# Optimization experiments

Measured on AMD Instinct MI355X. Metric: run time of the kernel, lower is better.

Reference implementation:

```python
import jax, jax.numpy as jnp
import numpy as np

B, N, DIM, H, DH, MLP, DEPTH = 32, 256, 384, 6, 64, 1536, 12
INNER = H * DH
LN_EPS = 1e-5
LS_INIT = 0.1  # LayerScale init_eps for depth <= 18


def setup_inputs() -> dict:
    key = jax.random.key(0)
    ks = jax.random.split(key, 10)
    f = lambda k, shape, s=0.02: jax.random.normal(k, shape, jnp.float32) * s
    return {
        "x": jax.random.normal(ks[0], (B, N, DIM), jnp.float32),
        "ln1_g": jnp.ones((DEPTH, DIM), jnp.float32),
        "ln1_b": jnp.zeros((DEPTH, DIM), jnp.float32),
        "wq": f(ks[1], (DEPTH, DIM, INNER)),
        "wkv": f(ks[2], (DEPTH, DIM, 2 * INNER)),
        "scale": jnp.full((DEPTH, H), DH ** -0.5, jnp.float32),  # learned per-head scale
        "mix_pre": f(ks[3], (DEPTH, H, H), 1.0),   # torch.randn init
        "mix_post": f(ks[4], (DEPTH, H, H), 1.0),
        "wo": f(ks[5], (DEPTH, INNER, DIM)),
        "bo": jnp.zeros((DEPTH, DIM), jnp.float32),
        "ls1": jnp.full((DEPTH, DIM), LS_INIT, jnp.float32),
        "ln2_g": jnp.ones((DEPTH, DIM), jnp.float32),
        "ln2_b": jnp.zeros((DEPTH, DIM), jnp.float32),
        "w1": f(ks[6], (DEPTH, DIM, MLP)),
        "b1": jnp.zeros((DEPTH, MLP), jnp.float32),
        "w2": f(ks[7], (DEPTH, MLP, DIM)),
        "b2": jnp.zeros((DEPTH, DIM), jnp.float32),
        "ls2": jnp.full((DEPTH, DIM), LS_INIT, jnp.float32),
    }


def _layernorm(x, g, b):
    mu = jnp.mean(x, axis=-1, keepdims=True)
    var = jnp.mean(jnp.square(x - mu), axis=-1, keepdims=True)
    return (x - mu) * jax.lax.rsqrt(var + LN_EPS) * g + b


def reference(x, ln1_g, ln1_b, wq, wkv, scale, mix_pre, mix_post, wo, bo, ls1,
              ln2_g, ln2_b, w1, b1, w2, b2, ls2):
    diag = jnp.eye(N, dtype=bool)  # self-attention diagonal mask

    def block(x, p):
        (g1, bb1, wq_, wkv_, sc, mp, mq, wo_, bo_, l1,
         g2, bb2, w1_, b1_, w2_, b2_, l2) = p
        # --- talking-heads attention (PreNorm + LayerScale + residual) ---
        y = _layernorm(x, g1, bb1)
        q = (y @ wq_).reshape(B, N, H, DH).transpose(0, 2, 1, 3)       # b h n d
        kv = y @ wkv_
        k, v = jnp.split(kv, 2, axis=-1)
        k = k.reshape(B, N, H, DH).transpose(0, 2, 1, 3)
        v = v.reshape(B, N, H, DH).transpose(0, 2, 1, 3)
        dots = jnp.einsum('bhid,bhjd->bhij', q, k) * sc[None, :, None, None]
        dots = jnp.einsum('bhij,hg->bgij', dots, mp)                   # pre-softmax head mix
        dots = jnp.where(diag, -jnp.inf, dots)                         # mask self positions
        attn = jax.nn.softmax(dots, axis=-1)
        attn = jnp.einsum('bhij,hg->bgij', attn, mq)                   # post-softmax head mix
        o = jnp.einsum('bhij,bhjd->bhid', attn, v)
        o = o.transpose(0, 2, 1, 3).reshape(B, N, INNER) @ wo_ + bo_
        x = o * l1 + x
        # --- FFN (PreNorm + LayerScale + residual) ---
        y2 = _layernorm(x, g2, bb2)
        h = jax.nn.gelu(y2 @ w1_ + b1_, approximate=False)
        x = (h @ w2_ + b2_) * l2 + x
        return x, None

    params = (ln1_g, ln1_b, wq, wkv, scale, mix_pre, mix_post, wo, bo, ls1,
              ln2_g, ln2_b, w1, b1, w2, b2, ls2)
    x, _ = jax.lax.scan(block, x, params)
    return x
```

## Files before the change

kernel.cpp:

```cpp
#include <hip/hip_runtime.h>
#include <hip/hip_bf16.h>
#include <math.h>

#define B_ 32
#define N_ 256
#define DIM_ 384
#define H_ 6
#define DH_ 64
#define INNER_ 384
#define MLP_ 1536
#define DEPTH_ 12
#define T_ (B_ * N_)

typedef __bf16 bf16x8 __attribute__((ext_vector_type(8)));
typedef __bf16 bf16x4 __attribute__((ext_vector_type(4)));
typedef float f32x4 __attribute__((ext_vector_type(4)));

#define WQKV_OFF 0
#define WO_OFF   (1152 * 384)
#define W1_OFF   (WO_OFF + 384 * 384)
#define W2_OFF   (W1_OFF + 1536 * 384)
#define WBUF_ELEMS (W2_OFF + 384 * 1536)

__global__ __launch_bounds__(256) void convert_w(
    const float* __restrict__ wq, const float* __restrict__ wkv,
    const float* __restrict__ wo, const float* __restrict__ w1,
    const float* __restrict__ w2, __bf16* __restrict__ wbuf)
{
    __shared__ float til[64][65];
    int t = blockIdx.x;
    int lane = threadIdx.x & 63, seg = threadIdx.x >> 6;
    const float* src; __bf16* dst;
    int Ns, sc, dK, dR, k0;
    if (t < 108) {
        int nt = t / 6, kt = t % 6;
        int n0 = nt * 64; k0 = kt * 64;
        dst = wbuf + WQKV_OFF; dK = 384; dR = n0;
        if (n0 < 384) { src = wq;  Ns = 384; sc = n0; }
        else          { src = wkv; Ns = 768; sc = n0 - 384; }
    } else if (t < 144) {
        int u = t - 108; int nt = u / 6, kt = u % 6;
        src = wo; Ns = 384; sc = nt * 64;
        dst = wbuf + WO_OFF; dK = 384; dR = nt * 64; k0 = kt * 64;
    } else if (t < 288) {
        int u = t - 144; int nt = u / 6, kt = u % 6;
        src = w1; Ns = 1536; sc = nt * 64;
        dst = wbuf + W1_OFF; dK = 384; dR = nt * 64; k0 = kt * 64;
    } else {
        int u = t - 288; int nt = u / 24, kt = u % 24;
        src = w2; Ns = 384; sc = nt * 64;
        dst = wbuf + W2_OFF; dK = 1536; dR = nt * 64; k0 = kt * 64;
    }
    #pragma unroll
    for (int r = 0; r < 16; ++r) {
        int i = seg * 16 + r;
        til[i][lane] = src[(size_t)(k0 + i) * Ns + sc + lane];
    }
    __syncthreads();
    #pragma unroll
    for (int r = 0; r < 16; ++r) {
        int i = seg * 16 + r;
        dst[(size_t)(dR + i) * dK + k0 + lane] = (__bf16)til[lane][i];
    }
}

__global__ __launch_bounds__(64) void ln1w(
    const float* __restrict__ x, const float* __restrict__ g,
    const float* __restrict__ b, __bf16* __restrict__ y)
{
    size_t row = blockIdx.x;
    int lane = threadIdx.x;
    const float* xr = x + row * DIM_;
    float v[6];
    #pragma unroll
    for (int s = 0; s < 6; ++s) v[s] = xr[lane + 64 * s];
    float sum = 0.f;
    #pragma unroll
    for (int s = 0; s < 6; ++s) sum += v[s];
    #pragma unroll
    for (int o = 32; o > 0; o >>= 1) sum += __shfl_xor(sum, o);
    float mu = sum * (1.0f / DIM_);
    float var = 0.f;
    #pragma unroll
    for (int s = 0; s < 6; ++s) { float d = v[s] - mu; var += d * d; }
    #pragma unroll
    for (int o = 32; o > 0; o >>= 1) var += __shfl_xor(var, o);
    float rs = rsqrtf(var * (1.0f / DIM_) + 1e-5f);
    __bf16* yr = y + row * DIM_;
    #pragma unroll
    for (int s = 0; s < 6; ++s) {
        int e = lane + 64 * s;
        yr[e] = (__bf16)((v[s] - mu) * rs * g[e] + b[e]);
    }
}

#define LDK 40

template<int MODE, int K>
__global__ __launch_bounds__(256) void gemm128(
    const __bf16* __restrict__ A, const __bf16* __restrict__ Bt,
    const float* __restrict__ bias, const float* __restrict__ ls,
    float* __restrict__ xf, __bf16* __restrict__ out,
    __bf16* __restrict__ oq, __bf16* __restrict__ ok, __bf16* __restrict__ ov,
    int Nn)
{
    __shared__ __bf16 sA[2][128 * LDK];
    __shared__ __bf16 sB[2][128 * LDK];
    int id = blockIdx.x;
    int g = id & 7, j = id >> 3;
    int bm = (g + ((j & 7) << 3)) << 7;
    int bn = (j >> 3) << 7;
    int tid = threadIdx.x;
    int lane = tid & 63, wid = tid >> 6;
    int wm = (wid & 1) * 64, wn = (wid >> 1) * 64;
    int fm = lane & 15, fq = lane >> 4;

    f32x4 acc[4][4] = {};

    int sr = tid >> 1, sh = (tid & 1) << 4;
    const __bf16* aSrc = A + (size_t)(bm + sr) * K + sh;
    const __bf16* bSrc = Bt + (size_t)(bn + sr) * K + sh;
    int soff = sr * LDK + sh;

    constexpr int nIter = K >> 5;

    {
        bf16x8 a0 = *(const bf16x8*)(aSrc);
        bf16x8 a1 = *(const bf16x8*)(aSrc + 8);
        bf16x8 b0 = *(const bf16x8*)(bSrc);
        bf16x8 b1 = *(const bf16x8*)(bSrc + 8);
        *(bf16x8*)&sA[0][soff]     = a0;
        *(bf16x8*)&sA[0][soff + 8] = a1;
        *(bf16x8*)&sB[0][soff]     = b0;
        *(bf16x8*)&sB[0][soff + 8] = b1;
    }
    bf16x8 pa0 = *(const bf16x8*)(aSrc + 32);
    bf16x8 pa1 = *(const bf16x8*)(aSrc + 40);
    bf16x8 pb0 = *(const bf16x8*)(bSrc + 32);
    bf16x8 pb1 = *(const bf16x8*)(bSrc + 40);
    __syncthreads();

    #pragma unroll
    for (int i = 0; i < nIter; ++i) {
        int cur = i & 1, nxt = cur ^ 1;
        bf16x8 af[4], bf[4];
        #pragma unroll
        for (int ii = 0; ii < 4; ++ii)
            af[ii] = *(const bf16x8*)&sA[cur][(wm + ii * 16 + fm) * LDK + fq * 8];
        #pragma unroll
        for (int jj = 0; jj < 4; ++jj)
            bf[jj] = *(const bf16x8*)&sB[cur][(wn + jj * 16 + fm) * LDK + fq * 8];
        if (i + 1 < nIter) {
            *(bf16x8*)&sA[nxt][soff]     = pa0;
            *(bf16x8*)&sA[nxt][soff + 8] = pa1;
            *(bf16x8*)&sB[nxt][soff]     = pb0;
            *(bf16x8*)&sB[nxt][soff + 8] = pb1;
        }
        if (i + 2 < nIter) {
            int ko = (i + 2) << 5;
            pa0 = *(const bf16x8*)(aSrc + ko);
            pa1 = *(const bf16x8*)(aSrc + ko + 8);
            pb0 = *(const bf16x8*)(bSrc + ko);
            pb1 = *(const bf16x8*)(bSrc + ko + 8);
        }
        #pragma unroll
        for (int ii = 0; ii < 4; ++ii)
            #pragma unroll
            for (int jj = 0; jj < 4; ++jj)
                acc[ii][jj] = __builtin_amdgcn_mfma_f32_16x16x32_bf16(af[ii], bf[jj], acc[ii][jj], 0, 0, 0);
        if (i + 1 < nIter) __syncthreads();
    }

    #pragma unroll
    for (int jj = 0; jj < 4; ++jj) {
        int col = bn + wn + jj * 16 + fm;
        float bv = (MODE != 0) ? bias[col] : 0.0f;
        float lv = (MODE == 2) ? ls[col] : 0.0f;
        #pragma unroll
        for (int i = 0; i < 4; ++i) {
            #pragma unroll
            for (int r = 0; r < 4; ++r) {
                int row = bm + wm + i * 16 + fq * 4 + r;
                float v = acc[i][jj][r];
                if (MODE == 0) {
                    if (col < 384)      oq[(size_t)row * 384 + col] = (__bf16)v;
                    else if (col < 768) ok[(size_t)row * 384 + col - 384] = (__bf16)v;
                    else {
                        int bb = row >> 8, tj = row & 255;
                        ov[((size_t)bb * 384 + (col - 768)) * 256 + tj] = (__bf16)v;
                    }
                } else if (MODE == 1) {
                    v += bv;
                    v = 0.5f * v * (1.0f + erff(v * 0.70710678118f));
                    out[(size_t)row * Nn + col] = (__bf16)v;
                } else {
                    size_t idx = (size_t)row * Nn + col;
                    xf[idx] = (v + bv) * lv + xf[idx];
                }
            }
        }
    }
}

#define PAD_S 264

__global__ __launch_bounds__(384) void attn_mfma(
    const __bf16* __restrict__ q, const __bf16* __restrict__ kb,
    const __bf16* __restrict__ vT, const float* __restrict__ scale,
    const float* __restrict__ mp, const float* __restrict__ mq,
    __bf16* __restrict__ o)
{
    __shared__ __bf16 sbuf[96][PAD_S];
    __shared__ float smp[36], smq[36];

    int id = blockIdx.x;
    int b = (id & 7) + ((id >> 3) & 3) * 8;
    int i0 = (id >> 5) * 16;
    int tid = threadIdx.x;
    int lane = tid & 63, wid = tid >> 6;
    int fm = lane & 15, fq = lane >> 4;

    if (tid < 36) {
        smp[tid] = mp[tid] * scale[tid / 6];
        smq[tid] = mq[tid];
    }

    int h = wid;
    bf16x8 qf[2];
    #pragma unroll
    for (int ks = 0; ks < 2; ++ks)
        qf[ks] = *(const bf16x8*)&q[(size_t)(b * 256 + i0 + fm) * 384 + h * 64 + ks * 32 + fq * 8];
    #pragma unroll 4
    for (int jt = 0; jt < 16; ++jt) {
        f32x4 a = {};
        #pragma unroll
        for (int ks = 0; ks < 2; ++ks) {
            bf16x8 bf = *(const bf16x8*)&kb[(size_t)(b * 256 + jt * 16 + fm) * 384 + h * 64 + ks * 32 + fq * 8];
            a = __builtin_amdgcn_mfma_f32_16x16x32_bf16(qf[ks], bf, a, 0, 0, 0);
        }
        #pragma unroll
        for (int r = 0; r < 4; ++r)
            sbuf[h * 16 + fq * 4 + r][jt * 16 + fm] = (__bf16)a[r];
    }
    __syncthreads();

    for (int idx = tid; idx < 4096; idx += 384) {
        int qq = idx >> 8, jx = idx & 255;
        float sv[6], ovv[6];
        #pragma unroll
        for (int h2 = 0; h2 < 6; ++h2) sv[h2] = (float)sbuf[h2 * 16 + qq][jx];
        #pragma unroll
        for (int gg = 0; gg < 6; ++gg) {
            float r2 = 0.f;
            #pragma unroll
            for (int h2 = 0; h2 < 6; ++h2) r2 += sv[h2] * smp[h2 * 6 + gg];
            ovv[gg] = (jx == i0 + qq) ? -1e30f : r2;
        }
        #pragma unroll
        for (int gg = 0; gg < 6; ++gg) sbuf[gg * 16 + qq][jx] = (__bf16)ovv[gg];
    }
    __syncthreads();

    for (int rr = 0; rr < 16; ++rr) {
        int row = wid * 16 + rr;
        bf16x4 v4 = *(const bf16x4*)&sbuf[row][lane * 4];
        float v0 = (float)v4[0], v1 = (float)v4[1], v2 = (float)v4[2], v3 = (float)v4[3];
        float m = fmaxf(fmaxf(v0, v1), fmaxf(v2, v3));
        #pragma unroll
        for (int off = 32; off > 0; off >>= 1) m = fmaxf(m, __shfl_xor(m, off));
        float e0 = __expf(v0 - m), e1 = __expf(v1 - m), e2 = __expf(v2 - m), e3 = __expf(v3 - m);
        float s = e0 + e1 + e2 + e3;
        #pragma unroll
        for (int off = 32; off > 0; off >>= 1) s += __shfl_xor(s, off);
        float inv = 1.0f / s;
        bf16x4 w4 = { (__bf16)(e0 * inv), (__bf16)(e1 * inv), (__bf16)(e2 * inv), (__bf16)(e3 * inv) };
        *(bf16x4*)&sbuf[row][lane * 4] = w4;
    }
    __syncthreads();

    for (int idx = tid; idx < 4096; idx += 384) {
        int qq = idx >> 8, jx = idx & 255;
        float sv[6], ovv[6];
        #pragma unroll
        for (int h2 = 0; h2 < 6; ++h2) sv[h2] = (float)sbuf[h2 * 16 + qq][jx];
        #pragma unroll
        for (int gg = 0; gg < 6; ++gg) {
            float r2 = 0.f;
            #pragma unroll
            for (int h2 = 0; h2 < 6; ++h2) r2 += sv[h2] * smq[h2 * 6 + gg];
            ovv[gg] = r2;
        }
        #pragma unroll
        for (int gg = 0; gg < 6; ++gg) sbuf[gg * 16 + qq][jx] = (__bf16)ovv[gg];
    }
    __syncthreads();

    int gg = wid;
    f32x4 acco[4] = {};
    #pragma unroll
    for (int jc = 0; jc < 4; ++jc) {
        #pragma unroll
        for (int ks = 0; ks < 2; ++ks) {
            bf16x8 af = *(const bf16x8*)&sbuf[gg * 16 + fm][jc * 64 + ks * 32 + fq * 8];
            #pragma unroll
            for (int nt = 0; nt < 4; ++nt) {
                bf16x8 bf = *(const bf16x8*)&vT[(size_t)(b * 384 + gg * 64 + nt * 16 + fm) * 256 + jc * 64 + ks * 32 + fq * 8];
                acco[nt] = __builtin_amdgcn_mfma_f32_16x16x32_bf16(af, bf, acco[nt], 0, 0, 0);
            }
        }
    }
    #pragma unroll
    for (int nt = 0; nt < 4; ++nt)
        #pragma unroll
        for (int r = 0; r < 4; ++r)
            o[(size_t)(b * 256 + i0 + fq * 4 + r) * 384 + gg * 64 + nt * 16 + fm] = (__bf16)acco[nt][r];
}

extern "C" void kernel_launch(void* const* d_in, const int* in_sizes, int n_in,
                              void* d_out, int out_size, void* d_ws, size_t ws_size,
                              hipStream_t stream) {
    const float* x      = (const float*)d_in[0];
    const float* ln1_g  = (const float*)d_in[1];
    const float* ln1_b  = (const float*)d_in[2];
    const float* wq     = (const float*)d_in[3];
    const float* wkv    = (const float*)d_in[4];
    const float* scale  = (const float*)d_in[5];
    const float* mixp   = (const float*)d_in[6];
    const float* mixq   = (const float*)d_in[7];
    const float* wo     = (const float*)d_in[8];
    const float* bo     = (const float*)d_in[9];
    const float* ls1    = (const float*)d_in[10];
    const float* ln2_g  = (const float*)d_in[11];
    const float* ln2_b  = (const float*)d_in[12];
    const float* w1     = (const float*)d_in[13];
    const float* b1     = (const float*)d_in[14];
    const float* w2     = (const float*)d_in[15];
    const float* b2     = (const float*)d_in[16];
    const float* ls2    = (const float*)d_in[17];

    char* ws = (char*)d_ws;
    float*  xf = (float*)ws;                      ws += (size_t)T_ * DIM_ * 4;
    __bf16* y  = (__bf16*)ws;                     ws += (size_t)T_ * DIM_ * 2;
    __bf16* q  = (__bf16*)ws;                     ws += (size_t)T_ * DIM_ * 2;
    __bf16* kb = (__bf16*)ws;                     ws += (size_t)T_ * DIM_ * 2;
    __bf16* vT = (__bf16*)ws;                     ws += (size_t)T_ * DIM_ * 2;
    __bf16* o  = (__bf16*)ws;                     ws += (size_t)T_ * DIM_ * 2;
    __bf16* wbuf = (__bf16*)ws;                   ws += (size_t)WBUF_ELEMS * 2;
    __bf16* h  = q;

    size_t nBytes = (size_t)T_ * DIM_ * sizeof(float);
    hipMemcpyAsync(xf, x, nBytes, hipMemcpyDeviceToDevice, stream);

    for (int l = 0; l < DEPTH_; ++l) {
        convert_w<<<432, 256, 0, stream>>>(
            wq + (size_t)l * DIM_ * INNER_, wkv + (size_t)l * DIM_ * 2 * INNER_,
            wo + (size_t)l * INNER_ * DIM_, w1 + (size_t)l * DIM_ * MLP_,
            w2 + (size_t)l * MLP_ * DIM_, wbuf);

        ln1w<<<T_, 64, 0, stream>>>(xf, ln1_g + (size_t)l * DIM_, ln1_b + (size_t)l * DIM_, y);

        gemm128<0, 384><<<64 * 9, 256, 0, stream>>>(
            y, wbuf + WQKV_OFF, nullptr, nullptr, nullptr, nullptr,
            q, kb, vT, 1152);

        attn_mfma<<<512, 384, 0, stream>>>(
            q, kb, vT, scale + (size_t)l * H_,
            mixp + (size_t)l * H_ * H_, mixq + (size_t)l * H_ * H_, o);

        gemm128<2, 384><<<64 * 3, 256, 0, stream>>>(
            o, wbuf + WO_OFF, bo + (size_t)l * DIM_, ls1 + (size_t)l * DIM_,
            xf, nullptr, nullptr, nullptr, nullptr, DIM_);

        ln1w<<<T_, 64, 0, stream>>>(xf, ln2_g + (size_t)l * DIM_, ln2_b + (size_t)l * DIM_, y);

        gemm128<1, 384><<<64 * 12, 256, 0, stream>>>(
            y, wbuf + W1_OFF, b1 + (size_t)l * MLP_, nullptr,
            nullptr, h, nullptr, nullptr, nullptr, MLP_);

        gemm128<2, 1536><<<64 * 3, 256, 0, stream>>>(
            h, wbuf + W2_OFF, b2 + (size_t)l * DIM_, ls2 + (size_t)l * DIM_,
            xf, nullptr, nullptr, nullptr, nullptr, DIM_);
    }

    hipMemcpyAsync(d_out, xf, nBytes, hipMemcpyDeviceToDevice, stream);
}
```

Measured before the change: 2.000 ms.

## Store Q/K/V in MFMA fragment-tiled layout and vectorize head-mix loops

The QKV GEMM epilogue now writes Q, K and V into 16x32 tiles of 512 contiguous elements, laid out to match the MFMA operand fragments. The attention kernel can then read each fragment with contiguous loads instead of row-strided gathers. The two talking-heads mixing passes are also rewritten to process 8 bf16 elements per thread using vector LDS loads and stores. The trade-off is more scattered global stores in the GEMM epilogue, in exchange for coalesced reads in attention.

```diff
diff --git a/kernel.cpp b/kernel.cpp
--- a/kernel.cpp
+++ b/kernel.cpp
@@ -183,11 +183,18 @@
                 int row = bm + wm + i * 16 + fq * 4 + r;
                 float v = acc[i][jj][r];
                 if (MODE == 0) {
-                    if (col < 384)      oq[(size_t)row * 384 + col] = (__bf16)v;
-                    else if (col < 768) ok[(size_t)row * 384 + col - 384] = (__bf16)v;
-                    else {
-                        int bb = row >> 8, tj = row & 255;
-                        ov[((size_t)bb * 384 + (col - 768)) * 256 + tj] = (__bf16)v;
+                    int b = row >> 8, tok = row & 255;
+                    if (col < 768) {
+                        int d = (col < 384) ? col : col - 384;
+                        __bf16* dst = (col < 384) ? oq : ok;
+                        size_t idx = ((size_t)((b * 16 + (tok >> 4)) * 12 + (d >> 5))) * 512
+                                   + (tok & 15) * 32 + (d & 31);
+                        dst[idx] = (__bf16)v;
+                    } else {
+                        int d = col - 768;
+                        size_t idx = ((size_t)((b * 24 + (d >> 4)) * 8 + (tok >> 5))) * 512
+                                   + (d & 15) * 32 + (tok & 31);
+                        ov[idx] = (__bf16)v;
                     }
                 } else if (MODE == 1) {
                     v += bv;
@@ -205,7 +212,7 @@
 #define PAD_S 264
 
 __global__ __launch_bounds__(384) void attn_mfma(
-    const __bf16* __restrict__ q, const __bf16* __restrict__ kb,
+    const __bf16* __restrict__ qT, const __bf16* __restrict__ kT,
     const __bf16* __restrict__ vT, const float* __restrict__ scale,
     const float* __restrict__ mp, const float* __restrict__ mq,
     __bf16* __restrict__ o)
@@ -215,7 +222,8 @@
 
     int id = blockIdx.x;
     int b = (id & 7) + ((id >> 3) & 3) * 8;
-    int i0 = (id >> 5) * 16;
+    int itile = id >> 5;
+    int i0 = itile * 16;
     int tid = threadIdx.x;
     int lane = tid & 63, wid = tid >> 6;
     int fm = lane & 15, fq = lane >> 4;
@@ -226,16 +234,17 @@
     }
 
     int h = wid;
+    int felem = fm * 32 + fq * 8;
     bf16x8 qf[2];
     #pragma unroll
     for (int ks = 0; ks < 2; ++ks)
-        qf[ks] = *(const bf16x8*)&q[(size_t)(b * 256 + i0 + fm) * 384 + h * 64 + ks * 32 + fq * 8];
+        qf[ks] = *(const bf16x8*)&qT[((size_t)((b * 16 + itile) * 12 + h * 2 + ks)) * 512 + felem];
     #pragma unroll 4
     for (int jt = 0; jt < 16; ++jt) {
         f32x4 a = {};
         #pragma unroll
         for (int ks = 0; ks < 2; ++ks) {
-            bf16x8 bf = *(const bf16x8*)&kb[(size_t)(b * 256 + jt * 16 + fm) * 384 + h * 64 + ks * 32 + fq * 8];
+            bf16x8 bf = *(const bf16x8*)&kT[((size_t)((b * 16 + jt) * 12 + h * 2 + ks)) * 512 + felem];
             a = __builtin_amdgcn_mfma_f32_16x16x32_bf16(qf[ks], bf, a, 0, 0, 0);
         }
         #pragma unroll
@@ -244,20 +253,23 @@
     }
     __syncthreads();
 
-    for (int idx = tid; idx < 4096; idx += 384) {
-        int qq = idx >> 8, jx = idx & 255;
-        float sv[6], ovv[6];
-        #pragma unroll
-        for (int h2 = 0; h2 < 6; ++h2) sv[h2] = (float)sbuf[h2 * 16 + qq][jx];
+    for (int idx = tid; idx < 512; idx += 384) {
+        int qq = idx >> 5, jb = idx & 31;
+        bf16x8 sv[6];
+        #pragma unroll
+        for (int h2 = 0; h2 < 6; ++h2) sv[h2] = *(const bf16x8*)&sbuf[h2 * 16 + qq][jb * 8];
         #pragma unroll
         for (int gg = 0; gg < 6; ++gg) {
-            float r2 = 0.f;
+            bf16x8 w;
             #pragma unroll
-            for (int h2 = 0; h2 < 6; ++h2) r2 += sv[h2] * smp[h2 * 6 + gg];
-            ovv[gg] = (jx == i0 + qq) ? -1e30f : r2;
-        }
-        #pragma unroll
-        for (int gg = 0; gg < 6; ++gg) sbuf[gg * 16 + qq][jx] = (__bf16)ovv[gg];
+            for (int e = 0; e < 8; ++e) {
+                float r2 = 0.f;
+                #pragma unroll
+                for (int h2 = 0; h2 < 6; ++h2) r2 += (float)sv[h2][e] * smp[h2 * 6 + gg];
+                w[e] = (__bf16)((jb * 8 + e == i0 + qq) ? -1e30f : r2);
+            }
+            *(bf16x8*)&sbuf[gg * 16 + qq][jb * 8] = w;
+        }
     }
     __syncthreads();
 
@@ -278,20 +290,23 @@
     }
     __syncthreads();
 
-    for (int idx = tid; idx < 4096; idx += 384) {
-        int qq = idx >> 8, jx = idx & 255;
-        float sv[6], ovv[6];
-        #pragma unroll
-        for (int h2 = 0; h2 < 6; ++h2) sv[h2] = (float)sbuf[h2 * 16 + qq][jx];
+    for (int idx = tid; idx < 512; idx += 384) {
+        int qq = idx >> 5, jb = idx & 31;
+        bf16x8 sv[6];
+        #pragma unroll
+        for (int h2 = 0; h2 < 6; ++h2) sv[h2] = *(const bf16x8*)&sbuf[h2 * 16 + qq][jb * 8];
         #pragma unroll
         for (int gg = 0; gg < 6; ++gg) {
-            float r2 = 0.f;
+            bf16x8 w;
             #pragma unroll
-            for (int h2 = 0; h2 < 6; ++h2) r2 += sv[h2] * smq[h2 * 6 + gg];
-            ovv[gg] = r2;
-        }
-        #pragma unroll
-        for (int gg = 0; gg < 6; ++gg) sbuf[gg * 16 + qq][jx] = (__bf16)ovv[gg];
+            for (int e = 0; e < 8; ++e) {
+                float r2 = 0.f;
+                #pragma unroll
+                for (int h2 = 0; h2 < 6; ++h2) r2 += (float)sv[h2][e] * smq[h2 * 6 + gg];
+                w[e] = (__bf16)r2;
+            }
+            *(bf16x8*)&sbuf[gg * 16 + qq][jb * 8] = w;
+        }
     }
     __syncthreads();
 
@@ -304,7 +319,7 @@
             bf16x8 af = *(const bf16x8*)&sbuf[gg * 16 + fm][jc * 64 + ks * 32 + fq * 8];
             #pragma unroll
             for (int nt = 0; nt < 4; ++nt) {
-                bf16x8 bf = *(const bf16x8*)&vT[(size_t)(b * 384 + gg * 64 + nt * 16 + fm) * 256 + jc * 64 + ks * 32 + fq * 8];
+                bf16x8 bf = *(const bf16x8*)&vT[((size_t)((b * 24 + gg * 4 + nt) * 8 + jc * 2 + ks)) * 512 + felem];
                 acco[nt] = __builtin_amdgcn_mfma_f32_16x16x32_bf16(af, bf, acco[nt], 0, 0, 0);
             }
         }
@@ -341,12 +356,12 @@
     char* ws = (char*)d_ws;
     float*  xf = (float*)ws;                      ws += (size_t)T_ * DIM_ * 4;
     __bf16* y  = (__bf16*)ws;                     ws += (size_t)T_ * DIM_ * 2;
-    __bf16* q  = (__bf16*)ws;                     ws += (size_t)T_ * DIM_ * 2;
-    __bf16* kb = (__bf16*)ws;                     ws += (size_t)T_ * DIM_ * 2;
+    __bf16* qT = (__bf16*)ws;                     ws += (size_t)T_ * DIM_ * 2;
+    __bf16* kT = (__bf16*)ws;                     ws += (size_t)T_ * DIM_ * 2;
     __bf16* vT = (__bf16*)ws;                     ws += (size_t)T_ * DIM_ * 2;
     __bf16* o  = (__bf16*)ws;                     ws += (size_t)T_ * DIM_ * 2;
     __bf16* wbuf = (__bf16*)ws;                   ws += (size_t)WBUF_ELEMS * 2;
-    __bf16* h  = q;
+    __bf16* h  = qT;
 
     size_t nBytes = (size_t)T_ * DIM_ * sizeof(float);
     hipMemcpyAsync(xf, x, nBytes, hipMemcpyDeviceToDevice, stream);
@@ -361,10 +376,10 @@
 
         gemm128<0, 384><<<64 * 9, 256, 0, stream>>>(
             y, wbuf + WQKV_OFF, nullptr, nullptr, nullptr, nullptr,
-            q, kb, vT, 1152);
+            qT, kT, vT, 1152);
 
         attn_mfma<<<512, 384, 0, stream>>>(
-            q, kb, vT, scale + (size_t)l * H_,
+            qT, kT, vT, scale + (size_t)l * H_,
             mixp + (size_t)l * H_ * H_, mixq + (size_t)l * H_ * H_, o);
 
         gemm128<2, 384><<<64 * 3, 256, 0, stream>>>(
```

Result: slower. 2.047 ms (+2.3%).
